# Optimization experiments

Measured on AMD Instinct MI355X. Metric: run time of the kernel, lower is better.

## Reference

```python
import jax, jax.numpy as jnp
import numpy as np

B, D, N0, N1 = 2, 512, 2048, 2048
ATT_DIM, OUT_DIM, H = 512, 512, 8
HEAD_ATT = ATT_DIM // H   # 64
HEAD_OUT = OUT_DIM // H   # 64
TEMP = 1.0
MASK_FILL = -10000000.0


def setup_inputs() -> dict:
    key = jax.random.key(0)
    ks = jax.random.split(key, 12)
    s = 0.02
    return {
        "feats_query": jax.random.normal(ks[0], (B, D, N0), dtype=jnp.float32),
        "feats_key": jax.random.normal(ks[1], (B, D, N1), dtype=jnp.float32),
        "key_mask": jax.random.randint(ks[2], (B, 1, N1), 0, 2, dtype=jnp.int32),
        # 1x1 Conv1d weights == (out_ch, in_ch) matrices
        "Wq": jax.random.normal(ks[3], (ATT_DIM, D), dtype=jnp.float32) * s,
        "bq": jnp.zeros((ATT_DIM,), dtype=jnp.float32),
        "Wk": jax.random.normal(ks[4], (ATT_DIM, D), dtype=jnp.float32) * s,
        "bk": jnp.zeros((ATT_DIM,), dtype=jnp.float32),
        "Wf": jax.random.normal(ks[5], (OUT_DIM, D), dtype=jnp.float32) * s,
        "bf": jnp.zeros((OUT_DIM,), dtype=jnp.float32),
        "Wm": jax.random.normal(ks[6], (OUT_DIM, OUT_DIM), dtype=jnp.float32) * s,
        "bm": jnp.zeros((OUT_DIM,), dtype=jnp.float32),
        "ln_g": jnp.ones((OUT_DIM,), dtype=jnp.float32),
        "ln_b": jnp.zeros((OUT_DIM,), dtype=jnp.float32),
    }


def _conv1x1(W, b, x):  # x: (b, in, n) -> (b, out, n)
    return jnp.einsum('oi,bin->bon', W, x) + b[None, :, None]


def reference(feats_query, feats_key, key_mask, Wq, bq, Wk, bk, Wf, bf, Wm, bm, ln_g, ln_b):
    b = feats_query.shape[0]
    n0 = feats_query.shape[2]
    n1 = feats_key.shape[2]
    # projections; channel split is (head_dim, head_num) per torch reshape
    q = _conv1x1(Wq, bq, feats_query).reshape(b, HEAD_ATT, H, n0)
    k = _conv1x1(Wk, bk, feats_key).reshape(b, HEAD_ATT, H, n1)
    v = _conv1x1(Wf, bf, feats_key).reshape(b, HEAD_OUT, H, n1)
    # attention: scores scaled by head_att_dim ** 0.5 (dim = query.shape[1])
    scores = jnp.einsum('bdhn,bdhm->bhnm', q / TEMP, k) / (HEAD_ATT ** 0.5)
    mask = key_mask.reshape(b, 1, 1, n1)
    scores = jnp.where(mask == 0, MASK_FILL, scores)
    prob = jax.nn.softmax(scores, axis=-1)
    feats_out = jnp.einsum('bhnm,bdhm->bdhn', prob, v).reshape(b, HEAD_OUT * H, n0)
    feats_out = _conv1x1(Wm, bm, feats_out)
    feats_out = feats_out + feats_query  # skip connection
    # SpecialLayerNorm: layernorm over channel dim (permute 0,2,1 -> LN -> permute back)
    x = feats_out.transpose(0, 2, 1)  # (b, n0, c)
    mu = jnp.mean(x, axis=-1, keepdims=True)
    var = jnp.var(x, axis=-1, keepdims=True)
    x = (x - mu) / jnp.sqrt(var + 1e-5) * ln_g + ln_b
    return x.transpose(0, 2, 1)  # (b, c, n0)
```

## Files before the change

### kernel.cpp

```cpp
#include <hip/hip_runtime.h>
#include <hip/hip_bf16.h>


using bf16x8 = __attribute__((ext_vector_type(8))) __bf16;
using f32x4  = __attribute__((ext_vector_type(4))) float;
using f32x16 = __attribute__((ext_vector_type(16))) float;
using us8    = __attribute__((ext_vector_type(8))) unsigned short;
using u32x4  = __attribute__((ext_vector_type(4))) unsigned int;

__device__ __forceinline__ unsigned short f2b(float f) {
  unsigned int u = __builtin_bit_cast(unsigned int, f);
  u += 0x7fffu + ((u >> 16) & 1u);
  return (unsigned short)(u >> 16);
}
__device__ __forceinline__ float b2f(unsigned short s) {
  unsigned int u = ((unsigned int)s) << 16;
  return __builtin_bit_cast(float, u);
}
__device__ __forceinline__ unsigned int cvtpk(float lo, float hi) {
  unsigned int w;
  asm("v_cvt_pk_bf16_f32 %0, %1, %2" : "=v"(w) : "v"(lo), "v"(hi));
  return w;
}
__device__ __forceinline__ void gl_lds16(const void* g, void* l) {
  __builtin_amdgcn_global_load_lds((const __attribute__((address_space(1))) void*)g,
                                   (__attribute__((address_space(3))) void*)l, 16, 0, 0);
}

__global__ __launch_bounds__(256) void k_pre(
    const float* __restrict__ fq, const float* __restrict__ fk,
    const float* __restrict__ Wq, const float* __restrict__ Wk,
    const float* __restrict__ Wf, const float* __restrict__ Wm,
    const int* __restrict__ mask,
    unsigned short* __restrict__ xqt, unsigned short* __restrict__ xkt,
    unsigned short* __restrict__ wqb, unsigned short* __restrict__ wkb,
    unsigned short* __restrict__ wfb, unsigned short* __restrict__ wmb,
    float* __restrict__ biasf)
{
  const int id = blockIdx.x;
  const int t = threadIdx.x;
  __shared__ float tile[64][65];

  if (id < 1024) {
    const int which = id >> 9;
    const int b = (id >> 8) & 1;
    const int i0 = ((id >> 5) & 7) * 64;
    const int n0 = (id & 31) * 64;
    const float* __restrict__ src = which ? fk : fq;
    unsigned short* __restrict__ dst = which ? xkt : xqt;
    const int cl = t & 63, rw = t >> 6;
    #pragma unroll
    for (int rr = 0; rr < 16; ++rr) {
      int il = rr * 4 + rw;
      tile[il][cl] = src[((size_t)b * 512 + i0 + il) * 2048 + n0 + cl];
    }
    __syncthreads();
    #pragma unroll
    for (int rr = 0; rr < 16; ++rr) {
      int nl = rr * 4 + rw;
      dst[((size_t)b * 2048 + n0 + nl) * 512 + i0 + cl] = f2b(tile[cl][nl]);
    }
  } else if (id < 3072) {
    const int r = id - 1024;
    const int mat = r >> 9, cp = r & 511;
    if (mat < 3) {
      const float* W = (mat == 0) ? Wq : (mat == 1) ? Wk : Wf;
      unsigned short* O = (mat == 0) ? wqb : (mat == 1) ? wkb : wfb;
      const int orig = (cp & 63) * 8 + (cp >> 6);
      for (int j = t; j < 512; j += 256)
        O[cp * 512 + j] = f2b(W[orig * 512 + j]);
    } else {
      for (int j = t; j < 512; j += 256) {
        int h = j >> 6, d = j & 63;
        wmb[cp * 512 + j] = f2b(Wm[cp * 512 + d * 8 + h]);
      }
    }
  } else {
    const int r = id - 3072;
    if (r < 16) {
      int i = r * 256 + t;
      biasf[i] = mask[i] ? 0.f : -100000.f;
    }
  }
}

__global__ __launch_bounds__(256) void k_proj(
    const unsigned short* __restrict__ xqt, const unsigned short* __restrict__ xkt,
    const unsigned short* __restrict__ wqp, const unsigned short* __restrict__ wkp,
    const unsigned short* __restrict__ wfp,
    const float* __restrict__ bq, const float* __restrict__ bk, const float* __restrict__ bfv,
    unsigned short* __restrict__ Qb, unsigned short* __restrict__ Kb, unsigned short* __restrict__ VTb)
{
  const int lid = blockIdx.x;
  const int orig = (lid & 7) * 48 + (lid >> 3);
  const int z = orig >> 6;
  const int bid = orig & 63;
  const int b = z / 3, proj = z % 3;
  const int t = threadIdx.x, w = t >> 6, l = t & 63, q = l >> 4, m16 = l & 15;
  const int wm = w >> 1, wn = w & 1;

  __shared__ __attribute__((aligned(16))) unsigned short As[2][8192];
  __shared__ __attribute__((aligned(16))) unsigned short Bs[2][8192];

  const unsigned short* A;
  const unsigned short* Bt;
  int mt, nt_;
  if (proj < 2) {
    mt = bid >> 2; nt_ = bid & 3;
    A  = (proj == 0 ? xqt : xkt) + (size_t)b * 2048 * 512 + (size_t)mt * 128 * 512;
    Bt = (proj == 0 ? wqp : wkp) + (size_t)nt_ * 128 * 512;
  } else {
    mt = bid & 3; nt_ = bid >> 2;
    A  = wfp + (size_t)mt * 128 * 512;
    Bt = xkt + (size_t)b * 2048 * 512 + (size_t)nt_ * 128 * 512;
  }

  f32x4 acc[4][4];
  const f32x4 fz = {0.f, 0.f, 0.f, 0.f};
  #pragma unroll
  for (int mf = 0; mf < 4; ++mf)
    #pragma unroll
    for (int nf = 0; nf < 4; ++nf) acc[mf][nf] = fz;

#define PROJ_STAGE(BUF, KS)                                                          \
  {                                                                                  \
    _Pragma("unroll")                                                                \
    for (int c = 0; c < 4; ++c) {                                                    \
      int slot = c * 256 + t;                                                        \
      int row = slot >> 3, j = slot & 7;                                             \
      int jj = j ^ (row & 7);                                                        \
      gl_lds16(A  + (size_t)row * 512 + (KS) * 64 + jj * 8,                          \
               (char*)As[BUF] + (c * 256 + w * 64) * 16);                            \
      gl_lds16(Bt + (size_t)row * 512 + (KS) * 64 + jj * 8,                          \
               (char*)Bs[BUF] + (c * 256 + w * 64) * 16);                            \
    }                                                                                \
  }

  PROJ_STAGE(0, 0)
  asm volatile("s_waitcnt vmcnt(0)" ::: "memory");
  __syncthreads();

  for (int ks = 0; ks < 8; ++ks) {
    const int cur = ks & 1;
    if (ks < 7) PROJ_STAGE(cur ^ 1, ks + 1)
    #pragma unroll
    for (int kk = 0; kk < 2; ++kk) {
      bf16x8 av[4], bv[4];
      #pragma unroll
      for (int mf = 0; mf < 4; ++mf) {
        int row = wm * 64 + mf * 16 + m16;
        av[mf] = *(const bf16x8*)&As[cur][row * 64 + (((kk * 4 + q) ^ (row & 7)) << 3)];
      }
      #pragma unroll
      for (int nf = 0; nf < 4; ++nf) {
        int row = wn * 64 + nf * 16 + m16;
        bv[nf] = *(const bf16x8*)&Bs[cur][row * 64 + (((kk * 4 + q) ^ (row & 7)) << 3)];
      }
      #pragma unroll
      for (int mf = 0; mf < 4; ++mf)
        #pragma unroll
        for (int nf = 0; nf < 4; ++nf)
          acc[mf][nf] = __builtin_amdgcn_mfma_f32_16x16x32_bf16(av[mf], bv[nf], acc[mf][nf], 0, 0, 0);
    }
    if (ks < 7) {
      asm volatile("s_waitcnt vmcnt(0)" ::: "memory");
      __syncthreads();
    }
  }
#undef PROJ_STAGE

  const float QSCALE = 0.18033688011112042f;

  if (proj < 2) {
    const float* bias = (proj == 0) ? bq : bk;
    unsigned short* dst = (proj == 0) ? Qb : Kb;
    #pragma unroll
    for (int mf = 0; mf < 4; ++mf)
      #pragma unroll
      for (int nf = 0; nf < 4; ++nf)
        #pragma unroll
        for (int r = 0; r < 4; ++r) {
          int n  = mt * 128 + wm * 64 + mf * 16 + q * 4 + r;
          int cp = nt_ * 128 + wn * 64 + nf * 16 + m16;
          int h = cp >> 6, d = cp & 63;
          float v = acc[mf][nf][r] + bias[d * 8 + h];
          if (proj == 0) v *= QSCALE;
          dst[((size_t)(b * 8 + h) * 2048 + n) * 64 + d] = f2b(v);
        }
  } else {
    #pragma unroll
    for (int mf = 0; mf < 4; ++mf)
      #pragma unroll
      for (int nf = 0; nf < 4; ++nf)
        #pragma unroll
        for (int r = 0; r < 4; ++r) {
          int cp = mt * 128 + wm * 64 + mf * 16 + q * 4 + r;
          int n  = nt_ * 128 + wn * 64 + nf * 16 + m16;
          int h = cp >> 6, d = cp & 63;
          float v = acc[mf][nf][r] + bfv[d * 8 + h];
          VTb[((size_t)(b * 8 + h) * 64 + d) * 2048 + n] = f2b(v);
        }
  }
}

__global__ __launch_bounds__(256, 2) void k_attn2(
    const unsigned short* __restrict__ Qb, const unsigned short* __restrict__ Kb,
    const unsigned short* __restrict__ VTb, const float* __restrict__ biasf,
    unsigned short* __restrict__ OT)
{
  const int lid = blockIdx.x;
  const int orig = ((lid & 7) << 6) | (lid >> 3);
  const int bh = orig >> 5, b = bh >> 3, h = bh & 7;
  const int nt = orig & 31;
  const int t = threadIdx.x, w = t >> 6, l = t & 63;
  const int q31 = l & 31, hi = l >> 5;

  __shared__ __attribute__((aligned(16))) char lds_all[65536];
  char* kbuf = lds_all + w * 8192;
  char* vbuf = lds_all + 32768 + w * 8192;

  const unsigned short* Kp = Kb + (size_t)bh * (2048 * 64);
  const unsigned short* Vp = VTb + (size_t)bh * (64 * 2048);
  const float* brow = biasf + b * 2048;

  bf16x8 qfr[2][4];
  {
    const unsigned short* Qp = Qb + ((size_t)bh * 2048 + nt * 64) * 64;
    #pragma unroll
    for (int qf = 0; qf < 2; ++qf)
      #pragma unroll
      for (int tq = 0; tq < 4; ++tq)
        qfr[qf][tq] = *(const bf16x8*)&Qp[(qf * 32 + q31) * 64 + tq * 16 + hi * 8];
  }

  f32x16 oacc[2][2];
  #pragma unroll
  for (int i = 0; i < 2; ++i)
    #pragma unroll
    for (int j2 = 0; j2 < 2; ++j2)
      #pragma unroll
      for (int r = 0; r < 16; ++r) oacc[i][j2][r] = 0.f;
  float lpart[2] = {0.f, 0.f};

  const int kr3 = l >> 3, ks3 = l & 7;
  const int vr4 = l >> 2, vs2 = l & 3;

  {
    int kv0 = w * 32;
    #pragma unroll
    for (int j = 0; j < 4; ++j)
      gl_lds16(Kp + (size_t)(kv0 + j * 8 + kr3) * 64 + (ks3 ^ kr3) * 8, kbuf + j * 1024);
    #pragma unroll
    for (int j = 0; j < 4; ++j) {
      int d = j * 16 + vr4;
      gl_lds16(Vp + (size_t)d * 2048 + kv0 + (vs2 ^ (d & 3)) * 8, vbuf + j * 1024);
    }
  }

  #pragma unroll 2
  for (int i = 0; i < 16; ++i) {
    const int bufi = i & 1;
    const int kv0 = (w + 4 * i) * 32;

    float4 bias[4];
    #pragma unroll
    for (int g = 0; g < 4; ++g)
      bias[g] = *(const float4*)&brow[kv0 + g * 8 + hi * 4];

    if (i < 15) {
      const int kvn = (w + 4 * (i + 1)) * 32;
      char* kb2 = kbuf + (bufi ^ 1) * 4096;
      char* vb2 = vbuf + (bufi ^ 1) * 4096;
      #pragma unroll
      for (int j = 0; j < 4; ++j)
        gl_lds16(Kp + (size_t)(kvn + j * 8 + kr3) * 64 + (ks3 ^ kr3) * 8, kb2 + j * 1024);
      #pragma unroll
      for (int j = 0; j < 4; ++j) {
        int d = j * 16 + vr4;
        gl_lds16(Vp + (size_t)d * 2048 + kvn + (vs2 ^ (d & 3)) * 8, vb2 + j * 1024);
      }
      asm volatile("s_waitcnt vmcnt(8)" ::: "memory");
    } else {
      asm volatile("s_waitcnt vmcnt(0)" ::: "memory");
    }
    __builtin_amdgcn_sched_barrier(0);

    const char* kb = kbuf + bufi * 4096;
    const char* vb = vbuf + bufi * 4096;

    bf16x8 ak[4];
    #pragma unroll
    for (int tq = 0; tq < 4; ++tq)
      ak[tq] = *(const bf16x8*)(kb + q31 * 128 + ((((tq << 1) | hi) ^ (q31 & 7)) * 16));

    f32x16 sacc[2];
    #pragma unroll
    for (int qf = 0; qf < 2; ++qf)
      #pragma unroll
      for (int r = 0; r < 16; ++r) sacc[qf][r] = 0.f;
    __builtin_amdgcn_s_setprio(1);
    #pragma unroll
    for (int tq = 0; tq < 4; ++tq) {
      sacc[0] = __builtin_amdgcn_mfma_f32_32x32x16_bf16(ak[tq], qfr[0][tq], sacc[0], 0, 0, 0);
      sacc[1] = __builtin_amdgcn_mfma_f32_32x32x16_bf16(ak[tq], qfr[1][tq], sacc[1], 0, 0, 0);
    }
    __builtin_amdgcn_s_setprio(0);

    bf16x8 av[2][2];
    #pragma unroll
    for (int df = 0; df < 2; ++df)
      #pragma unroll
      for (int tt = 0; tt < 2; ++tt)
        av[df][tt] = *(const bf16x8*)(vb + (df * 32 + q31) * 64 + ((((tt << 1) | hi) ^ (q31 & 3)) * 16));

    #pragma unroll
    for (int qf = 0; qf < 2; ++qf) {
      float e[16];
      #pragma unroll
      for (int g = 0; g < 4; ++g) {
        e[g*4+0] = __builtin_amdgcn_exp2f(sacc[qf][g*4+0] + bias[g].x);
        e[g*4+1] = __builtin_amdgcn_exp2f(sacc[qf][g*4+1] + bias[g].y);
        e[g*4+2] = __builtin_amdgcn_exp2f(sacc[qf][g*4+2] + bias[g].z);
        e[g*4+3] = __builtin_amdgcn_exp2f(sacc[qf][g*4+3] + bias[g].w);
      }
      float s0 = 0.f;
      #pragma unroll
      for (int r = 0; r < 16; ++r) s0 += e[r];
      lpart[qf] += s0;

      unsigned int W[8];
      #pragma unroll
      for (int j = 0; j < 8; ++j) W[j] = cvtpk(e[2*j], e[2*j+1]);
      asm("v_permlane32_swap_b32 %0, %1" : "+v"(W[0]), "+v"(W[2]));
      asm("v_permlane32_swap_b32 %0, %1" : "+v"(W[1]), "+v"(W[3]));
      asm("v_permlane32_swap_b32 %0, %1" : "+v"(W[4]), "+v"(W[6]));
      asm("v_permlane32_swap_b32 %0, %1" : "+v"(W[5]), "+v"(W[7]));
      u32x4 lo4 = {W[0], W[1], W[2], W[3]};
      u32x4 hi4 = {W[4], W[5], W[6], W[7]};
      bf16x8 pb0 = __builtin_bit_cast(bf16x8, lo4);
      bf16x8 pb1 = __builtin_bit_cast(bf16x8, hi4);

      __builtin_amdgcn_s_setprio(1);
      oacc[0][qf] = __builtin_amdgcn_mfma_f32_32x32x16_bf16(av[0][0], pb0, oacc[0][qf], 0, 0, 0);
      oacc[0][qf] = __builtin_amdgcn_mfma_f32_32x32x16_bf16(av[0][1], pb1, oacc[0][qf], 0, 0, 0);
      oacc[1][qf] = __builtin_amdgcn_mfma_f32_32x32x16_bf16(av[1][0], pb0, oacc[1][qf], 0, 0, 0);
      oacc[1][qf] = __builtin_amdgcn_mfma_f32_32x32x16_bf16(av[1][1], pb1, oacc[1][qf], 0, 0, 0);
      __builtin_amdgcn_s_setprio(0);
    }
  }

  unsigned short* ot = (unsigned short*)kbuf;
  #pragma unroll
  for (int qf = 0; qf < 2; ++qf) {
    float ls = lpart[qf] + __shfl_xor(lpart[qf], 32);
    float rinv = __builtin_amdgcn_rcpf(ls);
    int qq = qf * 32 + q31;
    #pragma unroll
    for (int df = 0; df < 2; ++df)
      #pragma unroll
      for (int rg = 0; rg < 4; ++rg)
        #pragma unroll
        for (int pr = 0; pr < 2; ++pr) {
          int r0 = rg * 4 + pr * 2;
          unsigned int wv = cvtpk(oacc[df][qf][r0] * rinv, oacc[df][qf][r0 + 1] * rinv);
          *(unsigned int*)((char*)ot + qq * 128 + (((df * 4 + rg) ^ (qq & 7)) * 16) + hi * 8 + pr * 4) = wv;
        }
  }
  #pragma unroll
  for (int j = 0; j < 8; ++j) {
    int qq = j * 8 + (l >> 3);
    int sl = l & 7;
    us8 val = *(const us8*)((const char*)ot + qq * 128 + ((sl ^ (qq & 7)) * 16));
    *(us8*)&OT[((size_t)b * 2048 + nt * 64 + qq) * 512 + h * 64 + sl * 8] = val;
  }
}

__global__ __launch_bounds__(256) void k_out(
    const unsigned short* __restrict__ OT, const unsigned short* __restrict__ wmw,
    const float* __restrict__ bm, const float* __restrict__ fq,
    const float* __restrict__ g, const float* __restrict__ be,
    float* __restrict__ out)
{
  const int b = blockIdx.y;
  const int n0 = blockIdx.x * 32;
  const int t = threadIdx.x, w = t >> 6, l = t & 63, q = l >> 4, m16 = l & 15;

  __shared__ __attribute__((aligned(16))) unsigned short As[2][2048];
  __shared__ __attribute__((aligned(16))) unsigned short Bs[2][32768];
  __shared__ float ssum[4][32], ssq[4][32];

  f32x4 acc[2][8];
  const f32x4 fz = {0.f, 0.f, 0.f, 0.f};
  #pragma unroll
  for (int mf = 0; mf < 2; ++mf)
    #pragma unroll
    for (int nf = 0; nf < 8; ++nf) acc[mf][nf] = fz;

  const unsigned short* Abase = OT + ((size_t)b * 2048 + n0) * 512;
  const unsigned short* Bbase = wmw;

#define OUT_STAGE(BUF, KS)                                                          \
  {                                                                                 \
    { int row = t >> 3, j = t & 7;                                                  \
      gl_lds16(Abase + (size_t)row * 512 + (KS) * 64 + ((j ^ (row & 7)) * 8),       \
               (char*)As[BUF] + w * 1024); }                                        \
    _Pragma("unroll")                                                               \
    for (int c = 0; c < 16; ++c) {                                                  \
      int slot = c * 256 + t;                                                       \
      int row = slot >> 3, j = slot & 7;                                            \
      gl_lds16(Bbase + (size_t)row * 512 + (KS) * 64 + ((j ^ (row & 7)) * 8),       \
               (char*)Bs[BUF] + (c * 256 + w * 64) * 16);                           \
    }                                                                               \
  }

  OUT_STAGE(0, 0)
  asm volatile("s_waitcnt vmcnt(0)" ::: "memory");
  __syncthreads();

  for (int ks = 0; ks < 8; ++ks) {
    const int cur = ks & 1;
    if (ks < 7) OUT_STAGE(cur ^ 1, ks + 1)
    #pragma unroll
    for (int kk = 0; kk < 2; ++kk) {
      bf16x8 av[2];
      #pragma unroll
      for (int mf = 0; mf < 2; ++mf) {
        int row = mf * 16 + m16;
        av[mf] = *(const bf16x8*)((const char*)As[cur] + row * 128 + (((kk * 4 + q) ^ (row & 7)) * 16));
      }
      #pragma unroll
      for (int nf = 0; nf < 8; ++nf) {
        int row = w * 128 + nf * 16 + m16;
        bf16x8 bv = *(const bf16x8*)((const char*)Bs[cur] + row * 128 + (((kk * 4 + q) ^ (row & 7)) * 16));
        acc[0][nf] = __builtin_amdgcn_mfma_f32_16x16x32_bf16(av[0], bv, acc[0][nf], 0, 0, 0);
        acc[1][nf] = __builtin_amdgcn_mfma_f32_16x16x32_bf16(av[1], bv, acc[1][nf], 0, 0, 0);
      }
    }
    if (ks < 7) {
      asm volatile("s_waitcnt vmcnt(0)" ::: "memory");
      __syncthreads();
    }
  }
#undef OUT_STAGE

  float gv[8], bev[8], bmv[8];
  #pragma unroll
  for (int nf = 0; nf < 8; ++nf) {
    int c = w * 128 + nf * 16 + m16;
    gv[nf] = g[c]; bev[nf] = be[c]; bmv[nf] = bm[c];
  }
  #pragma unroll
  for (int mf = 0; mf < 2; ++mf)
    #pragma unroll
    for (int nf = 0; nf < 8; ++nf) {
      int c = w * 128 + nf * 16 + m16;
      f32x4 res = *(const f32x4*)&fq[((size_t)b * 512 + c) * 2048 + n0 + mf * 16 + q * 4];
      #pragma unroll
      for (int r = 0; r < 4; ++r)
        acc[mf][nf][r] += bmv[nf] + res[r];
    }
  #pragma unroll
  for (int mf = 0; mf < 2; ++mf)
    #pragma unroll
    for (int r = 0; r < 4; ++r) {
      float ps = 0.f, pss = 0.f;
      #pragma unroll
      for (int nf = 0; nf < 8; ++nf) {
        float v = acc[mf][nf][r];
        ps += v; pss += v * v;
      }
      ps += __shfl_xor(ps, 1); pss += __shfl_xor(pss, 1);
      ps += __shfl_xor(ps, 2); pss += __shfl_xor(pss, 2);
      ps += __shfl_xor(ps, 4); pss += __shfl_xor(pss, 4);
      ps += __shfl_xor(ps, 8); pss += __shfl_xor(pss, 8);
      if (m16 == 0) {
        ssum[w][mf * 16 + q * 4 + r] = ps;
        ssq[w][mf * 16 + q * 4 + r] = pss;
      }
    }
  __syncthreads();
  #pragma unroll
  for (int mf = 0; mf < 2; ++mf)
    #pragma unroll
    for (int r = 0; r < 4; ++r) {
      int nl = mf * 16 + q * 4 + r;
      float S  = ssum[0][nl] + ssum[1][nl] + ssum[2][nl] + ssum[3][nl];
      float SS = ssq[0][nl] + ssq[1][nl] + ssq[2][nl] + ssq[3][nl];
      float mu = S * (1.f / 512.f);
      float var = SS * (1.f / 512.f) - mu * mu;
      float rstd = rsqrtf(var + 1e-5f);
      #pragma unroll
      for (int nf = 0; nf < 8; ++nf)
        acc[mf][nf][r] = (acc[mf][nf][r] - mu) * rstd * gv[nf] + bev[nf];
    }
  #pragma unroll
  for (int mf = 0; mf < 2; ++mf)
    #pragma unroll
    for (int nf = 0; nf < 8; ++nf) {
      int c = w * 128 + nf * 16 + m16;
      *(f32x4*)&out[((size_t)b * 512 + c) * 2048 + n0 + mf * 16 + q * 4] = acc[mf][nf];
    }
}

extern "C" void kernel_launch(void* const* d_in, const int* in_sizes, int n_in,
                              void* d_out, int out_size, void* d_ws, size_t ws_size,
                              hipStream_t stream) {
  const float* fq  = (const float*)d_in[0];
  const float* fk  = (const float*)d_in[1];
  const int*   msk = (const int*)d_in[2];
  const float* Wq  = (const float*)d_in[3];
  const float* bq  = (const float*)d_in[4];
  const float* Wk  = (const float*)d_in[5];
  const float* bk  = (const float*)d_in[6];
  const float* Wf  = (const float*)d_in[7];
  const float* bfv = (const float*)d_in[8];
  const float* Wm  = (const float*)d_in[9];
  const float* bm  = (const float*)d_in[10];
  const float* lng = (const float*)d_in[11];
  const float* lnb = (const float*)d_in[12];
  float* out = (float*)d_out;

  char* ws = (char*)d_ws;
  const size_t MB = 1024 * 1024;
  unsigned short* xqt = (unsigned short*)(ws + 0 * MB);
  unsigned short* xkt = (unsigned short*)(ws + 4 * MB);
  unsigned short* wqb = (unsigned short*)(ws + 8 * MB);
  unsigned short* wkb = (unsigned short*)(ws + 8 * MB + 512 * 1024);
  unsigned short* wfb = (unsigned short*)(ws + 9 * MB);
  unsigned short* wmb = (unsigned short*)(ws + 9 * MB + 512 * 1024);
  unsigned short* Qb  = (unsigned short*)(ws + 10 * MB);
  unsigned short* Kb  = (unsigned short*)(ws + 14 * MB);
  unsigned short* VTb = (unsigned short*)(ws + 18 * MB);
  unsigned short* OTb = (unsigned short*)(ws + 22 * MB);
  float*          biasf = (float*)(ws + 26 * MB);

  hipLaunchKernelGGL(k_pre, dim3(3088), dim3(256), 0, stream,
                     fq, fk, Wq, Wk, Wf, Wm, msk, xqt, xkt, wqb, wkb, wfb, wmb, biasf);
  hipLaunchKernelGGL(k_proj, dim3(384), dim3(256), 0, stream,
                     xqt, xkt, wqb, wkb, wfb, bq, bk, bfv, Qb, Kb, VTb);
  hipLaunchKernelGGL(k_attn2, dim3(512), dim3(256), 0, stream, Qb, Kb, VTb, biasf, OTb);
  hipLaunchKernelGGL(k_out, dim3(64, 2), dim3(256), 0, stream,
                     OTb, wmb, bm, fq, lng, lnb, out);
}
```

Measured before the change: 72.57 us.

## Restructure attention to share K/V tiles across warps, with packed transpose stores

The attention kernel now uses 128-query blocks where each of the four warps owns 32 queries. All warps share block-wide double-buffered 64-key K/V tiles loaded cooperatively and synchronized with __syncthreads. Before, each warp streamed its own disjoint KV slice and covered 64 queries. Each K/V byte loaded into LDS is now reused by four times as many queries, and the grid halves to 256 blocks. The cost is a block barrier every iteration and possibly lower occupancy and parallelism. Separately, the pre-transpose stage writes two bf16 values per 32-bit store instead of one 16-bit store.

Result: slower. 89.76 us (+23.7%).

```diff
diff --git a/kernel.cpp b/kernel.cpp
--- a/kernel.cpp
+++ b/kernel.cpp
@@ -55,10 +55,13 @@
       tile[il][cl] = src[((size_t)b * 512 + i0 + il) * 2048 + n0 + cl];
     }
     __syncthreads();
-    #pragma unroll
-    for (int rr = 0; rr < 16; ++rr) {
-      int nl = rr * 4 + rw;
-      dst[((size_t)b * 2048 + n0 + nl) * 512 + i0 + cl] = f2b(tile[cl][nl]);
+    const int ci = (t & 31) * 2, rhalf = t >> 5;
+    #pragma unroll
+    for (int rr = 0; rr < 8; ++rr) {
+      int nl = rr * 8 + rhalf;
+      unsigned int v = (unsigned int)f2b(tile[ci][nl]) |
+                       ((unsigned int)f2b(tile[ci + 1][nl]) << 16);
+      *(unsigned int*)&dst[((size_t)b * 2048 + n0 + nl) * 512 + i0 + ci] = v;
     }
   } else if (id < 3072) {
     const int r = id - 1024;
@@ -203,130 +206,105 @@
   }
 }
 
-__global__ __launch_bounds__(256, 2) void k_attn2(
+__global__ __launch_bounds__(256) void k_attn3(
     const unsigned short* __restrict__ Qb, const unsigned short* __restrict__ Kb,
     const unsigned short* __restrict__ VTb, const float* __restrict__ biasf,
     unsigned short* __restrict__ OT)
 {
   const int lid = blockIdx.x;
-  const int orig = ((lid & 7) << 6) | (lid >> 3);
-  const int bh = orig >> 5, b = bh >> 3, h = bh & 7;
-  const int nt = orig & 31;
+  const int orig = (lid & 7) * 32 + (lid >> 3);
+  const int bh = orig >> 4, b = bh >> 3, h = bh & 7;
+  const int nt = orig & 15;
   const int t = threadIdx.x, w = t >> 6, l = t & 63;
   const int q31 = l & 31, hi = l >> 5;
 
-  __shared__ __attribute__((aligned(16))) char lds_all[65536];
-  char* kbuf = lds_all + w * 8192;
-  char* vbuf = lds_all + 32768 + w * 8192;
+  __shared__ __attribute__((aligned(16))) char lds_all[32768];
+  char* kb0 = lds_all;
+  char* vb0 = lds_all + 16384;
 
   const unsigned short* Kp = Kb + (size_t)bh * (2048 * 64);
   const unsigned short* Vp = VTb + (size_t)bh * (64 * 2048);
   const float* brow = biasf + b * 2048;
-
-  bf16x8 qfr[2][4];
+  const int qbase = nt * 128 + w * 32;
+
+  bf16x8 qfr[4];
   {
-    const unsigned short* Qp = Qb + ((size_t)bh * 2048 + nt * 64) * 64;
-    #pragma unroll
-    for (int qf = 0; qf < 2; ++qf)
+    const unsigned short* Qp = Qb + ((size_t)bh * 2048 + qbase) * 64;
+    #pragma unroll
+    for (int tq = 0; tq < 4; ++tq)
+      qfr[tq] = *(const bf16x8*)&Qp[q31 * 64 + tq * 16 + hi * 8];
+  }
+
+  f32x16 z16;
+  #pragma unroll
+  for (int r = 0; r < 16; ++r) z16[r] = 0.f;
+  f32x16 oacc[2];
+  oacc[0] = z16; oacc[1] = z16;
+  float lpart = 0.f;
+
+  const int srow = t >> 3, sslot = t & 7;
+
+#define ATTN_STAGE(BUF, KV0)                                                          \
+  {                                                                                   \
+    _Pragma("unroll")                                                                 \
+    for (int c = 0; c < 2; ++c) {                                                     \
+      int row = c * 32 + srow;                                                        \
+      gl_lds16(Kp + (size_t)((KV0) + row) * 64 + (sslot ^ (row & 7)) * 8,             \
+               kb0 + (BUF) * 8192 + c * 4096 + w * 1024);                             \
+      gl_lds16(Vp + (size_t)row * 2048 + (KV0) + (sslot ^ (row & 7)) * 8,             \
+               vb0 + (BUF) * 8192 + c * 4096 + w * 1024);                             \
+    }                                                                                 \
+  }
+
+  ATTN_STAGE(0, 0)
+  asm volatile("s_waitcnt vmcnt(0)" ::: "memory");
+  __syncthreads();
+
+  for (int i = 0; i < 32; ++i) {
+    const int cur = i & 1;
+    const int kv0 = i * 64;
+
+    if (i < 31) ATTN_STAGE(cur ^ 1, kv0 + 64)
+
+    const char* kb = kb0 + cur * 8192;
+    const char* vb = vb0 + cur * 8192;
+
+    float4 bias[2][4];
+    #pragma unroll
+    for (int ks = 0; ks < 2; ++ks)
+      #pragma unroll
+      for (int g = 0; g < 4; ++g)
+        bias[ks][g] = *(const float4*)&brow[kv0 + ks * 32 + g * 8 + hi * 4];
+
+    #pragma unroll
+    for (int ks = 0; ks < 2; ++ks) {
+      bf16x8 ak[4];
       #pragma unroll
       for (int tq = 0; tq < 4; ++tq)
-        qfr[qf][tq] = *(const bf16x8*)&Qp[(qf * 32 + q31) * 64 + tq * 16 + hi * 8];
-  }
-
-  f32x16 oacc[2][2];
-  #pragma unroll
-  for (int i = 0; i < 2; ++i)
-    #pragma unroll
-    for (int j2 = 0; j2 < 2; ++j2)
-      #pragma unroll
-      for (int r = 0; r < 16; ++r) oacc[i][j2][r] = 0.f;
-  float lpart[2] = {0.f, 0.f};
-
-  const int kr3 = l >> 3, ks3 = l & 7;
-  const int vr4 = l >> 2, vs2 = l & 3;
-
-  {
-    int kv0 = w * 32;
-    #pragma unroll
-    for (int j = 0; j < 4; ++j)
-      gl_lds16(Kp + (size_t)(kv0 + j * 8 + kr3) * 64 + (ks3 ^ kr3) * 8, kbuf + j * 1024);
-    #pragma unroll
-    for (int j = 0; j < 4; ++j) {
-      int d = j * 16 + vr4;
-      gl_lds16(Vp + (size_t)d * 2048 + kv0 + (vs2 ^ (d & 3)) * 8, vbuf + j * 1024);
-    }
-  }
-
-  #pragma unroll 2
-  for (int i = 0; i < 16; ++i) {
-    const int bufi = i & 1;
-    const int kv0 = (w + 4 * i) * 32;
-
-    float4 bias[4];
-    #pragma unroll
-    for (int g = 0; g < 4; ++g)
-      bias[g] = *(const float4*)&brow[kv0 + g * 8 + hi * 4];
-
-    if (i < 15) {
-      const int kvn = (w + 4 * (i + 1)) * 32;
-      char* kb2 = kbuf + (bufi ^ 1) * 4096;
-      char* vb2 = vbuf + (bufi ^ 1) * 4096;
-      #pragma unroll
-      for (int j = 0; j < 4; ++j)
-        gl_lds16(Kp + (size_t)(kvn + j * 8 + kr3) * 64 + (ks3 ^ kr3) * 8, kb2 + j * 1024);
-      #pragma unroll
-      for (int j = 0; j < 4; ++j) {
-        int d = j * 16 + vr4;
-        gl_lds16(Vp + (size_t)d * 2048 + kvn + (vs2 ^ (d & 3)) * 8, vb2 + j * 1024);
-      }
-      asm volatile("s_waitcnt vmcnt(8)" ::: "memory");
-    } else {
-      asm volatile("s_waitcnt vmcnt(0)" ::: "memory");
-    }
-    __builtin_amdgcn_sched_barrier(0);
-
-    const char* kb = kbuf + bufi * 4096;
-    const char* vb = vbuf + bufi * 4096;
-
-    bf16x8 ak[4];
-    #pragma unroll
-    for (int tq = 0; tq < 4; ++tq)
-      ak[tq] = *(const bf16x8*)(kb + q31 * 128 + ((((tq << 1) | hi) ^ (q31 & 7)) * 16));
-
-    f32x16 sacc[2];
-    #pragma unroll
-    for (int qf = 0; qf < 2; ++qf)
-      #pragma unroll
-      for (int r = 0; r < 16; ++r) sacc[qf][r] = 0.f;
-    __builtin_amdgcn_s_setprio(1);
-    #pragma unroll
-    for (int tq = 0; tq < 4; ++tq) {
-      sacc[0] = __builtin_amdgcn_mfma_f32_32x32x16_bf16(ak[tq], qfr[0][tq], sacc[0], 0, 0, 0);
-      sacc[1] = __builtin_amdgcn_mfma_f32_32x32x16_bf16(ak[tq], qfr[1][tq], sacc[1], 0, 0, 0);
-    }
-    __builtin_amdgcn_s_setprio(0);
-
-    bf16x8 av[2][2];
-    #pragma unroll
-    for (int df = 0; df < 2; ++df)
-      #pragma unroll
-      for (int tt = 0; tt < 2; ++tt)
-        av[df][tt] = *(const bf16x8*)(vb + (df * 32 + q31) * 64 + ((((tt << 1) | hi) ^ (q31 & 3)) * 16));
-
-    #pragma unroll
-    for (int qf = 0; qf < 2; ++qf) {
+        ak[tq] = *(const bf16x8*)(kb + (ks * 32 + q31) * 128 + ((((tq << 1) | hi) ^ (q31 & 7)) * 16));
+
+      f32x16 sacc;
+      __builtin_amdgcn_s_setprio(1);
+      sacc = __builtin_amdgcn_mfma_f32_32x32x16_bf16(ak[0], qfr[0], z16, 0, 0, 0);
+      #pragma unroll
+      for (int tq = 1; tq < 4; ++tq)
+        sacc = __builtin_amdgcn_mfma_f32_32x32x16_bf16(ak[tq], qfr[tq], sacc, 0, 0, 0);
+      __builtin_amdgcn_s_setprio(0);
+
       float e[16];
       #pragma unroll
       for (int g = 0; g < 4; ++g) {
-        e[g*4+0] = __builtin_amdgcn_exp2f(sacc[qf][g*4+0] + bias[g].x);
-        e[g*4+1] = __builtin_amdgcn_exp2f(sacc[qf][g*4+1] + bias[g].y);
-        e[g*4+2] = __builtin_amdgcn_exp2f(sacc[qf][g*4+2] + bias[g].z);
-        e[g*4+3] = __builtin_amdgcn_exp2f(sacc[qf][g*4+3] + bias[g].w);
-      }
-      float s0 = 0.f;
-      #pragma unroll
-      for (int r = 0; r < 16; ++r) s0 += e[r];
-      lpart[qf] += s0;
+        e[g*4+0] = __builtin_amdgcn_exp2f(sacc[g*4+0] + bias[ks][g].x);
+        e[g*4+1] = __builtin_amdgcn_exp2f(sacc[g*4+1] + bias[ks][g].y);
+        e[g*4+2] = __builtin_amdgcn_exp2f(sacc[g*4+2] + bias[ks][g].z);
+        e[g*4+3] = __builtin_amdgcn_exp2f(sacc[g*4+3] + bias[ks][g].w);
+      }
+      {
+        float s0 = e[0]+e[1], s1 = e[2]+e[3], s2 = e[4]+e[5], s3 = e[6]+e[7];
+        float s4 = e[8]+e[9], s5 = e[10]+e[11], s6 = e[12]+e[13], s7 = e[14]+e[15];
+        float t0 = s0+s1, t1 = s2+s3, t2 = s4+s5, t3 = s6+s7;
+        lpart += (t0+t1) + (t2+t3);
+      }
 
       unsigned int W[8];
       #pragma unroll
@@ -340,21 +318,28 @@
       bf16x8 pb0 = __builtin_bit_cast(bf16x8, lo4);
       bf16x8 pb1 = __builtin_bit_cast(bf16x8, hi4);
 
+      bf16x8 av00 = *(const bf16x8*)(vb + q31 * 128 + (((((ks*2+0) << 1) | hi) ^ (q31 & 7)) * 16));
+      bf16x8 av01 = *(const bf16x8*)(vb + q31 * 128 + (((((ks*2+1) << 1) | hi) ^ (q31 & 7)) * 16));
+      bf16x8 av10 = *(const bf16x8*)(vb + (32 + q31) * 128 + (((((ks*2+0) << 1) | hi) ^ (q31 & 7)) * 16));
+      bf16x8 av11 = *(const bf16x8*)(vb + (32 + q31) * 128 + (((((ks*2+1) << 1) | hi) ^ (q31 & 7)) * 16));
+
       __builtin_amdgcn_s_setprio(1);
-      oacc[0][qf] = __builtin_amdgcn_mfma_f32_32x32x16_bf16(av[0][0], pb0, oacc[0][qf], 0, 0, 0);
-      oacc[0][qf] = __builtin_amdgcn_mfma_f32_32x32x16_bf16(av[0][1], pb1, oacc[0][qf], 0, 0, 0);
-      oacc[1][qf] = __builtin_amdgcn_mfma_f32_32x32x16_bf16(av[1][0], pb0, oacc[1][qf], 0, 0, 0);
-      oacc[1][qf] = __builtin_amdgcn_mfma_f32_32x32x16_bf16(av[1][1], pb1, oacc[1][qf], 0, 0, 0);
+      oacc[0] = __builtin_amdgcn_mfma_f32_32x32x16_bf16(av00, pb0, oacc[0], 0, 0, 0);
+      oacc[0] = __builtin_amdgcn_mfma_f32_32x32x16_bf16(av01, pb1, oacc[0], 0, 0, 0);
+      oacc[1] = __builtin_amdgcn_mfma_f32_32x32x16_bf16(av10, pb0, oacc[1], 0, 0, 0);
+      oacc[1] = __builtin_amdgcn_mfma_f32_32x32x16_bf16(av11, pb1, oacc[1], 0, 0, 0);
       __builtin_amdgcn_s_setprio(0);
     }
-  }
-
-  unsigned short* ot = (unsigned short*)kbuf;
-  #pragma unroll
-  for (int qf = 0; qf < 2; ++qf) {
-    float ls = lpart[qf] + __shfl_xor(lpart[qf], 32);
+
+    asm volatile("s_waitcnt vmcnt(0)" ::: "memory");
+    __syncthreads();
+  }
+#undef ATTN_STAGE
+
+  unsigned short* ot = (unsigned short*)(lds_all + w * 4096);
+  {
+    float ls = lpart + __shfl_xor(lpart, 32);
     float rinv = __builtin_amdgcn_rcpf(ls);
-    int qq = qf * 32 + q31;
     #pragma unroll
     for (int df = 0; df < 2; ++df)
       #pragma unroll
@@ -362,16 +347,16 @@
         #pragma unroll
         for (int pr = 0; pr < 2; ++pr) {
           int r0 = rg * 4 + pr * 2;
-          unsigned int wv = cvtpk(oacc[df][qf][r0] * rinv, oacc[df][qf][r0 + 1] * rinv);
-          *(unsigned int*)((char*)ot + qq * 128 + (((df * 4 + rg) ^ (qq & 7)) * 16) + hi * 8 + pr * 4) = wv;
+          unsigned int wv = cvtpk(oacc[df][r0] * rinv, oacc[df][r0 + 1] * rinv);
+          *(unsigned int*)((char*)ot + q31 * 128 + (((df * 4 + rg) ^ (q31 & 7)) * 16) + hi * 8 + pr * 4) = wv;
         }
   }
   #pragma unroll
-  for (int j = 0; j < 8; ++j) {
+  for (int j = 0; j < 4; ++j) {
     int qq = j * 8 + (l >> 3);
     int sl = l & 7;
     us8 val = *(const us8*)((const char*)ot + qq * 128 + ((sl ^ (qq & 7)) * 16));
-    *(us8*)&OT[((size_t)b * 2048 + nt * 64 + qq) * 512 + h * 64 + sl * 8] = val;
+    *(us8*)&OT[((size_t)b * 2048 + qbase + qq) * 512 + h * 64 + sl * 8] = val;
   }
 }
 
@@ -538,7 +523,7 @@
                      fq, fk, Wq, Wk, Wf, Wm, msk, xqt, xkt, wqb, wkb, wfb, wmb, biasf);
   hipLaunchKernelGGL(k_proj, dim3(384), dim3(256), 0, stream,
                      xqt, xkt, wqb, wkb, wfb, bq, bk, bfv, Qb, Kb, VTb);
-  hipLaunchKernelGGL(k_attn2, dim3(512), dim3(256), 0, stream, Qb, Kb, VTb, biasf, OTb);
+  hipLaunchKernelGGL(k_attn3, dim3(256), dim3(256), 0, stream, Qb, Kb, VTb, biasf, OTb);
   hipLaunchKernelGGL(k_out, dim3(64, 2), dim3(256), 0, stream,
                      OTb, wmb, bm, fq, lng, lnb, out);
 }
```
